# Performance work log

Measured on AMD Instinct MI355X. Metric: run time of the kernel, lower is better.

## Reference

```python
import jax, jax.numpy as jnp
import numpy as np

BS = 256      # number of graphs
NODES = 128   # nodes per graph (equal-size segments)
N = BS * NODES
D = 64        # node feature dim
C = 64        # codebook atoms
K = 32        # support points per atom


def setup_inputs() -> dict:
    key = jax.random.key(0)
    k1, k2 = jax.random.split(key)
    x = jax.random.normal(k1, (N, D), dtype=jnp.float32)
    atoms = jax.random.normal(k2, (C, K, D), dtype=jnp.float32)
    batch = jnp.repeat(jnp.arange(BS, dtype=jnp.int64), NODES)  # sorted graph ids
    return {"x": x, "atoms": atoms, "batch": batch, "bs": BS}


def _sq_dists(a, b):
    # a: [..., n, D], b: [..., m, D] -> [..., n, m] squared euclidean distances
    an = jnp.sum(a * a, axis=-1)
    bn = jnp.sum(b * b, axis=-1)
    ab = jnp.einsum('...nd,...md->...nm', a, b)
    return an[..., :, None] + bn[..., None, :] - 2.0 * ab


def reference(x, atoms, batch, bs):
    # Faithful vectorized version of GINSWDSingleModel._mmd_distances with
    # gamma = 1/D (default). Assumes equal-size graphs (batch = repeat(arange(bs), n)).
    Nn, Dd = x.shape
    Cc, Kk, _ = atoms.shape
    n = Nn // bs
    gamma = 1.0 / Dd
    xg = x.reshape(bs, n, Dd)                      # [bs, n, D]

    # k_xx: within-graph RBF kernel mean, per graph -> [bs]
    k_xx = jnp.exp(-gamma * _sq_dists(xg, xg)).mean(axis=(1, 2))

    # k_yy: within-atom kernel mean, per atom -> [C]
    k_yy = jnp.exp(-gamma * _sq_dists(atoms, atoms)).mean(axis=(1, 2))

    # k_xy: cross kernel mean between graph nodes and atom points -> [bs, C]
    xn = jnp.sum(xg * xg, axis=-1)                 # [bs, n]
    an = jnp.sum(atoms * atoms, axis=-1)           # [C, K]
    xa = jnp.einsum('bnd,ckd->bnck', xg, atoms)    # [bs, n, C, K]
    dxy = xn[:, :, None, None] + an[None, None, :, :] - 2.0 * xa
    k_xy = jnp.exp(-gamma * dxy).mean(axis=(1, 3))  # [bs, C]

    return k_xx[:, None] + k_yy[None, :] - 2.0 * k_xy
```

## Files before the change

kernel.cpp:

```cpp
#include <hip/hip_runtime.h>
#include <hip/hip_bf16.h>


constexpr int   NODES = 128;
constexpr int   DD    = 64;
constexpr int   CC    = 64;
constexpr int   KK    = 32;
constexpr float GAMMA = 1.0f / 64.0f;
constexpr float LOG2E = 1.4426950408889634f;
constexpr float C1    = 2.0f * GAMMA * LOG2E;
constexpr float GL    = GAMMA * LOG2E;

typedef __attribute__((ext_vector_type(8)))  short short8;
typedef __attribute__((ext_vector_type(16))) float f32x16;

#define MFMA(a, b, c) __builtin_amdgcn_mfma_f32_32x32x16_bf16((a), (b), (c), 0, 0, 0)

__device__ __forceinline__ float fexp2(float x) {
#if __has_builtin(__builtin_amdgcn_exp2f)
    return __builtin_amdgcn_exp2f(x);
#else
    return exp2f(x);
#endif
}

__device__ __forceinline__ unsigned short f2bf(float f) {
    union { float f; unsigned int u; } a; a.f = f;
    unsigned int u = a.u;
    return (unsigned short)((u + 0x7FFFu + ((u >> 16) & 1u)) >> 16);
}

__device__ __forceinline__ void gl16(const void* g, void* l) {
    __builtin_amdgcn_global_load_lds(
        (const __attribute__((address_space(1))) char*)g,
        (__attribute__((address_space(3))) char*)l, 16, 0, 0);
}

__global__ __launch_bounds__(256) void prep_atoms(const float* __restrict__ atoms,
                                                  short8* __restrict__ bfrag,
                                                  float* __restrict__ can,
                                                  float* __restrict__ kyy) {
    const int c = blockIdx.x, t = threadIdx.x;
    __shared__ float a[KK][DD + 1];
    __shared__ float an[KK];
    __shared__ float wred[4];

    const float* ac = atoms + (size_t)c * KK * DD;
    for (int i = t; i < KK * DD; i += 256) a[i >> 6][i & 63] = ac[i];
    __syncthreads();

    if (t < KK) {
        float s = 0.f;
#pragma unroll
        for (int d = 0; d < DD; ++d) s = fmaf(a[t][d], a[t][d], s);
        an[t] = s;
        can[c * KK + t] = -GL * s;
    }
    __syncthreads();

    {
        const int wv = t >> 6, l = t & 63;
        const int kp = l & 31, khh = l >> 5;
        short8 h;
#pragma unroll
        for (int j = 0; j < 8; ++j)
            h[j] = (short)f2bf(C1 * a[kp][wv * 16 + khh * 8 + j]);
        bfrag[(size_t)c * 256 + wv * 64 + l] = h;
    }

    {
        const int i = t >> 3, j0 = (t & 7) * 4;
        float s0 = 0, s1 = 0, s2 = 0, s3 = 0;
        for (int d = 0; d < DD; ++d) {
            const float aid = a[i][d];
            s0 = fmaf(aid, a[j0 + 0][d], s0);
            s1 = fmaf(aid, a[j0 + 1][d], s1);
            s2 = fmaf(aid, a[j0 + 2][d], s2);
            s3 = fmaf(aid, a[j0 + 3][d], s3);
        }
        const float ani = an[i];
        float s = fexp2(-GL * (ani + an[j0 + 0] - 2.f * s0))
                + fexp2(-GL * (ani + an[j0 + 1] - 2.f * s1))
                + fexp2(-GL * (ani + an[j0 + 2] - 2.f * s2))
                + fexp2(-GL * (ani + an[j0 + 3] - 2.f * s3));
#pragma unroll
        for (int off = 32; off; off >>= 1) s += __shfl_xor(s, off);
        if ((t & 63) == 0) wred[t >> 6] = s;
    }
    __syncthreads();
    if (t == 0) kyy[c] = (wred[0] + wred[1] + wred[2] + wred[3]) * (1.0f / (KK * KK));
}

__global__ __launch_bounds__(256, 4) void mmd_fused(const float* __restrict__ x,
                                                    const short8* __restrict__ bfrag,
                                                    const float* __restrict__ can,
                                                    const float* __restrict__ kyy,
                                                    float* __restrict__ out) {
    const int bid = blockIdx.x, b = bid >> 2, cq = bid & 3;
    const int t = threadIdx.x, w = t >> 6, l = t & 63;
    const int l31 = l & 31, kh = l >> 5;

    __shared__ short8 Bb[2][4][256];
    __shared__ float  part16[4][20][16];
    __shared__ float  nl[NODES];
    __shared__ float  sxy_s[16];
    __shared__ float  kxx_s;

    float v[32];
    {
        const float* xr = x + ((size_t)(b * NODES + w * 32 + l31)) * DD + kh * 8;
#pragma unroll
        for (int kt = 0; kt < 4; ++kt) {
            const float4 p0 = *reinterpret_cast<const float4*>(xr + kt * 16);
            const float4 p1 = *reinterpret_cast<const float4*>(xr + kt * 16 + 4);
            v[kt*8+0]=p0.x; v[kt*8+1]=p0.y; v[kt*8+2]=p0.z; v[kt*8+3]=p0.w;
            v[kt*8+4]=p1.x; v[kt*8+5]=p1.y; v[kt*8+6]=p1.z; v[kt*8+7]=p1.w;
        }
    }
    float xn = 0.f;
#pragma unroll
    for (int i = 0; i < 32; ++i) xn = fmaf(v[i], v[i], xn);
    xn += __shfl_xor(xn, 32);
    if (l < 32) nl[w * 32 + l] = -GL * xn;

    short8 A[4];
#pragma unroll
    for (int kt = 0; kt < 4; ++kt) {
        short8 h;
#pragma unroll
        for (int j = 0; j < 8; ++j) h[j] = (short)f2bf(v[kt * 8 + j]);
        A[kt] = h;
        Bb[0][w][kt * 64 + l] = h;
    }

    float cav[16];
#pragma unroll
    for (int j = 0; j < 16; ++j) cav[j] = can[(cq * 16 + j) * KK + l31];

    __syncthreads();

    f32x16 cx;
    {
        const float* nb = &nl[w * 32 + 4 * kh];
#pragma unroll
        for (int q = 0; q < 4; ++q) {
            const float4 vq = *reinterpret_cast<const float4*>(nb + 8 * q);
            cx[4*q+0] = vq.x; cx[4*q+1] = vq.y; cx[4*q+2] = vq.z; cx[4*q+3] = vq.w;
        }
    }

    const short8* bq = bfrag + (size_t)(cq * 16) * 256;

#pragma unroll
    for (int s = 0; s < 5; ++s) {
        if (s < 4) {
            const short8* src = bq + (size_t)(s * 4 + w) * 256;
#pragma unroll
            for (int q = 0; q < 4; ++q)
                gl16(src + q * 64 + l, &Bb[(s + 1) & 1][w][q * 64]);
        }
#pragma unroll
        for (int p = 0; p < 4; ++p) {
            short8 Bt[4];
#pragma unroll
            for (int kt = 0; kt < 4; ++kt) Bt[kt] = Bb[s & 1][p][kt * 64 + l];

            float ssum;
            if (s == 0) {
                f32x16 acc = {};
#pragma unroll
                for (int kt = 0; kt < 4; ++kt) acc = MFMA(A[kt], Bt[kt], acc);
                const float ec0 = fexp2(nl[p * 32 + l31]);
                float sa = 0.f, sb = 0.f;
#pragma unroll
                for (int r = 0; r < 16; r += 2) {
                    sa += fexp2(fmaf(C1, acc[r],     cx[r]));
                    sb += fexp2(fmaf(C1, acc[r + 1], cx[r + 1]));
                }
                ssum = (sa + sb) * ec0;
            } else {
                const int j = (s - 1) * 4 + p;
                f32x16 acc;
#pragma unroll
                for (int r = 0; r < 16; ++r) acc[r] = cx[r] + cav[j];
#pragma unroll
                for (int kt = 0; kt < 4; ++kt) acc = MFMA(A[kt], Bt[kt], acc);
                float sa = 0.f, sb = 0.f;
#pragma unroll
                for (int r = 0; r < 16; r += 2) {
                    sa += fexp2(acc[r]);
                    sb += fexp2(acc[r + 1]);
                }
                ssum = sa + sb;
            }
            ssum += __shfl_xor(ssum, 32);
            ssum += __shfl_xor(ssum, 16);
            if (l < 16) part16[w][s * 4 + p][l] = ssum;
        }
        __syncthreads();
    }

    {
        const int o = t >> 4, g = t & 15;
        float s1 = part16[0][4 + o][g] + part16[1][4 + o][g]
                 + part16[2][4 + o][g] + part16[3][4 + o][g];
        s1 += __shfl_xor(s1, 8);
        s1 += __shfl_xor(s1, 4);
        s1 += __shfl_xor(s1, 2);
        s1 += __shfl_xor(s1, 1);
        if (g == 0) sxy_s[o] = s1;
    }
    if (t < 16) {
        float kx = 0.f;
#pragma unroll
        for (int ww = 0; ww < 4; ++ww)
#pragma unroll
            for (int q = 0; q < 4; ++q) kx += part16[ww][q][t];
        kx += __shfl_xor(kx, 8);
        kx += __shfl_xor(kx, 4);
        kx += __shfl_xor(kx, 2);
        kx += __shfl_xor(kx, 1);
        if (t == 0) kxx_s = kx;
    }
    __syncthreads();
    if (t < 16) {
        out[(size_t)b * CC + cq * 16 + t] =
            kxx_s * (1.0f / 16384.0f) + kyy[cq * 16 + t] - sxy_s[t] * (1.0f / 2048.0f);
    }
}

extern "C" void kernel_launch(void* const* d_in, const int* in_sizes, int n_in,
                              void* d_out, int out_size, void* d_ws, size_t ws_size,
                              hipStream_t stream) {
    const float* x     = (const float*)d_in[0];
    const float* atoms = (const float*)d_in[1];
    float* out = (float*)d_out;

    char* ws = (char*)d_ws;
    short8* bfrag = (short8*)(ws);
    float*  can   = (float*) (ws + 262144);
    float*  kyy   = (float*) (ws + 270336);

    prep_atoms<<<dim3(CC),   dim3(256), 0, stream>>>(atoms, bfrag, can, kyy);
    mmd_fused <<<dim3(1024), dim3(256), 0, stream>>>(x, bfrag, can, kyy, out);
}
```

Baseline: 29.37 us.

## Load atom B-fragments directly into registers with double buffering instead of LDS

The atom B-fragments are now read straight from global memory into a two-slot register double buffer, replacing the LDS staging through global_load_lds and the per-stage barriers. The k_xx pass runs first using an LDS exchange of the node fragments, and the atom norm terms move into shared memory instead of 16 registers per thread. This is meant to remove the five __syncthreads and the LDS traffic on the cross-term loop. The cost is that every wave fetches each atom's fragments from global or L2 separately, and the register footprint changes.

```diff
diff --git a/kernel.cpp b/kernel.cpp
--- a/kernel.cpp
+++ b/kernel.cpp
@@ -30,12 +30,6 @@
     return (unsigned short)((u + 0x7FFFu + ((u >> 16) & 1u)) >> 16);
 }
 
-__device__ __forceinline__ void gl16(const void* g, void* l) {
-    __builtin_amdgcn_global_load_lds(
-        (const __attribute__((address_space(1))) char*)g,
-        (__attribute__((address_space(3))) char*)l, 16, 0, 0);
-}
-
 __global__ __launch_bounds__(256) void prep_atoms(const float* __restrict__ atoms,
                                                   short8* __restrict__ bfrag,
                                                   float* __restrict__ can,
@@ -100,9 +94,10 @@
     const int t = threadIdx.x, w = t >> 6, l = t & 63;
     const int l31 = l & 31, kh = l >> 5;
 
-    __shared__ short8 Bb[2][4][256];
+    __shared__ short8 Axch[4][256];
     __shared__ float  part16[4][20][16];
     __shared__ float  nl[NODES];
+    __shared__ float  cavl[16][32];
     __shared__ float  sxy_s[16];
     __shared__ float  kxx_s;
 
@@ -130,12 +125,10 @@
 #pragma unroll
         for (int j = 0; j < 8; ++j) h[j] = (short)f2bf(v[kt * 8 + j]);
         A[kt] = h;
-        Bb[0][w][kt * 64 + l] = h;
-    }
-
-    float cav[16];
-#pragma unroll
-    for (int j = 0; j < 16; ++j) cav[j] = can[(cq * 16 + j) * KK + l31];
+        Axch[w][kt * 64 + l] = h;
+    }
+
+    for (int i = t; i < 512; i += 256) cavl[i >> 5][i & 31] = can[cq * 512 + i];
 
     __syncthreads();
 
@@ -149,56 +142,60 @@
         }
     }
 
+#pragma unroll
+    for (int p = 0; p < 4; ++p) {
+        short8 Bt[4];
+#pragma unroll
+        for (int kt = 0; kt < 4; ++kt) Bt[kt] = Axch[p][kt * 64 + l];
+        f32x16 acc = {};
+#pragma unroll
+        for (int kt = 0; kt < 4; ++kt) acc = MFMA(A[kt], Bt[kt], acc);
+        const float ec0 = fexp2(nl[p * 32 + l31]);
+        float sa = 0.f, sb = 0.f;
+#pragma unroll
+        for (int r = 0; r < 16; r += 2) {
+            sa += fexp2(fmaf(C1, acc[r],     cx[r]));
+            sb += fexp2(fmaf(C1, acc[r + 1], cx[r + 1]));
+        }
+        float ssum = (sa + sb) * ec0;
+        ssum += __shfl_xor(ssum, 32);
+        ssum += __shfl_xor(ssum, 16);
+        if (l < 16) part16[w][p][l] = ssum;
+    }
+
     const short8* bq = bfrag + (size_t)(cq * 16) * 256;
-
-#pragma unroll
-    for (int s = 0; s < 5; ++s) {
-        if (s < 4) {
-            const short8* src = bq + (size_t)(s * 4 + w) * 256;
-#pragma unroll
-            for (int q = 0; q < 4; ++q)
-                gl16(src + q * 64 + l, &Bb[(s + 1) & 1][w][q * 64]);
-        }
-#pragma unroll
-        for (int p = 0; p < 4; ++p) {
-            short8 Bt[4];
-#pragma unroll
-            for (int kt = 0; kt < 4; ++kt) Bt[kt] = Bb[s & 1][p][kt * 64 + l];
-
-            float ssum;
-            if (s == 0) {
-                f32x16 acc = {};
-#pragma unroll
-                for (int kt = 0; kt < 4; ++kt) acc = MFMA(A[kt], Bt[kt], acc);
-                const float ec0 = fexp2(nl[p * 32 + l31]);
-                float sa = 0.f, sb = 0.f;
-#pragma unroll
-                for (int r = 0; r < 16; r += 2) {
-                    sa += fexp2(fmaf(C1, acc[r],     cx[r]));
-                    sb += fexp2(fmaf(C1, acc[r + 1], cx[r + 1]));
-                }
-                ssum = (sa + sb) * ec0;
-            } else {
-                const int j = (s - 1) * 4 + p;
-                f32x16 acc;
-#pragma unroll
-                for (int r = 0; r < 16; ++r) acc[r] = cx[r] + cav[j];
-#pragma unroll
-                for (int kt = 0; kt < 4; ++kt) acc = MFMA(A[kt], Bt[kt], acc);
-                float sa = 0.f, sb = 0.f;
-#pragma unroll
-                for (int r = 0; r < 16; r += 2) {
-                    sa += fexp2(acc[r]);
-                    sb += fexp2(acc[r + 1]);
-                }
-                ssum = sa + sb;
-            }
-            ssum += __shfl_xor(ssum, 32);
-            ssum += __shfl_xor(ssum, 16);
-            if (l < 16) part16[w][s * 4 + p][l] = ssum;
-        }
-        __syncthreads();
-    }
+    short8 Breg[2][4];
+#pragma unroll
+    for (int kt = 0; kt < 4; ++kt) {
+        Breg[0][kt] = bq[kt * 64 + l];
+        Breg[1][kt] = bq[256 + kt * 64 + l];
+    }
+#pragma unroll
+    for (int j = 0; j < 16; ++j) {
+        const float ca = cavl[j][l31];
+        f32x16 acc;
+#pragma unroll
+        for (int r = 0; r < 16; ++r) acc[r] = cx[r] + ca;
+#pragma unroll
+        for (int kt = 0; kt < 4; ++kt) acc = MFMA(A[kt], Breg[j & 1][kt], acc);
+        if (j < 14) {
+#pragma unroll
+            for (int kt = 0; kt < 4; ++kt)
+                Breg[j & 1][kt] = bq[(size_t)(j + 2) * 256 + kt * 64 + l];
+        }
+        float sa = 0.f, sb = 0.f;
+#pragma unroll
+        for (int r = 0; r < 16; r += 2) {
+            sa += fexp2(acc[r]);
+            sb += fexp2(acc[r + 1]);
+        }
+        float ssum = sa + sb;
+        ssum += __shfl_xor(ssum, 32);
+        ssum += __shfl_xor(ssum, 16);
+        if (l < 16) part16[w][4 + j][l] = ssum;
+    }
+
+    __syncthreads();
 
     {
         const int o = t >> 4, g = t & 15;
```

Result: no change. 29.31 us, median of 2 (-0.2%).
